# Kernel optimization log

Hardware: AMD Instinct MI355X
Metric: run time of the kernel (lower is better)

Reference implementation:

```python
import jax, jax.numpy as jnp
import numpy as np

B, D_IN, H, HV, A, E, HW = 16384, 512, 512, 256, 32, 8, 512

def _lin(key, fan_in, fan_out):
    k1, k2 = jax.random.split(key)
    s = 1.0 / np.sqrt(fan_in)
    W = jax.random.uniform(k1, (fan_in, fan_out), minval=-s, maxval=s, dtype=jnp.float32)
    b = jax.random.uniform(k2, (fan_out,), minval=-s, maxval=s, dtype=jnp.float32)
    return W, b

def _stack(key, n, fan_in, fan_out):
    Ws, bs = [], []
    for k in jax.random.split(key, n):
        W, b = _lin(k, fan_in, fan_out)
        Ws.append(W); bs.append(b)
    return jnp.stack(Ws), jnp.stack(bs)

def setup_inputs() -> dict:
    key = jax.random.key(0)
    ks = jax.random.split(key, 16)
    x = jax.random.normal(ks[0], (B, D_IN), dtype=jnp.float32)
    # stacked expert policy nets: in->H, H->H, H->A (tanh)
    Wp0, bp0 = _stack(ks[1], E, D_IN, H)
    Wp1, bp1 = _stack(ks[2], E, H, H)
    Wmu, bmu = _stack(ks[3], E, H, A)
    # stacked expert value nets (hardcoded 256 hidden in source): in->256, 256->256, 256->1
    Wv0, bv0 = _stack(ks[4], E, D_IN, HV)
    Wv1, bv1 = _stack(ks[5], E, HV, HV)
    Wv, bv = _stack(ks[6], E, HV, 1)
    # gating net: in->HW, HW->HW, HW->E, softmax
    Ww0, bw0 = _lin(ks[7], D_IN, HW)
    Ww1, bw1 = _lin(ks[8], HW, HW)
    Wwo, bwo = _lin(ks[9], HW, E)
    return dict(x=x, Wp0=Wp0, bp0=bp0, Wp1=Wp1, bp1=bp1, Wmu=Wmu, bmu=bmu,
                Wv0=Wv0, bv0=bv0, Wv1=Wv1, bv1=bv1, Wv=Wv, bv=bv,
                Ww0=Ww0, bw0=bw0, Ww1=Ww1, bw1=bw1, Wwo=Wwo, bwo=bwo)

def reference(x, Wp0, bp0, Wp1, bp1, Wmu, bmu, Wv0, bv0, Wv1, bv1, Wv, bv,
              Ww0, bw0, Ww1, bw1, Wwo, bwo):
    # experts as one grouped/batched GEMM over axis e
    h = jax.nn.relu(jnp.einsum('bi,eih->ebh', x, Wp0) + bp0[:, None, :])      # [E,B,H]
    h = jax.nn.relu(jnp.einsum('ebh,ehk->ebk', h, Wp1) + bp1[:, None, :])
    actions = jnp.tanh(jnp.einsum('ebh,eha->eba', h, Wmu) + bmu[:, None, :])  # [E,B,A]
    # per-expert values
    g = jax.nn.relu(jnp.einsum('bi,eih->ebh', x, Wv0) + bv0[:, None, :])      # [E,B,HV]
    g = jax.nn.relu(jnp.einsum('ebh,ehk->ebk', g, Wv1) + bv1[:, None, :])
    values = jnp.einsum('ebh,eho->ebo', g, Wv) + bv[:, None, :]               # [E,B,1]
    # gating network + softmax
    u = jax.nn.relu(x @ Ww0 + bw0)
    u = jax.nn.relu(u @ Ww1 + bw1)
    w = jax.nn.softmax(u @ Wwo + bwo, axis=-1)                                # [B,E]
    # Categorical(w).sample() with a fixed key, then per-row gather of values
    pis = jax.random.categorical(jax.random.key(42), jnp.log(w), axis=-1)     # [B] int
    v = values[pis, jnp.arange(values.shape[1])]                              # [B,1]
    return actions, v, w
```

## Files before the change

kernel.cpp:

```cpp
#include <hip/hip_runtime.h>


typedef float   f32x4 __attribute__((ext_vector_type(4)));
typedef _Float16 f16;
typedef _Float16 f16x4 __attribute__((ext_vector_type(4)));
typedef _Float16 f16x8 __attribute__((ext_vector_type(8)));

typedef __attribute__((address_space(1))) unsigned int gas_u32;
typedef __attribute__((address_space(3))) unsigned int las_u32;

__device__ __forceinline__ void gl_lds16(const void* g, void* l) {
  __builtin_amdgcn_global_load_lds((gas_u32*)g, (las_u32*)l, 16, 0, 0);
}

__device__ __forceinline__ int xcd_swz(int b, int G) {
  int q = G >> 3, r = G & 7;
  int x = b & 7, y = b >> 3;
  return (x < r ? x * (q + 1) : r * (q + 1) + (x - r) * q) + y;
}

template<int BM, int BN, int WM, int WN, int EPI>
__global__ __launch_bounds__(256, 2) void gemm2_kernel(
    const f16* __restrict__ A, const f16* __restrict__ BT,
    const float* __restrict__ bias, void* __restrict__ Cv,
    const int K, const long long sAe, const long long sCe,
    const int mT, const int nInner, const int eShift)
{
  constexpr int FM = WM / 16, FN = WN / 16;
  constexpr int WAVES_N = BN / WN;
  __shared__ __align__(16) char sm[(BM + BN) * 128];
  char* Ash = sm;
  char* Bsh = sm + BM * 128;

  const int tid = threadIdx.x;
  const int lane = tid & 63;
  const int wid = tid >> 6;

  const int L = xcd_swz(blockIdx.x, gridDim.x);
  const int nIn = L % nInner;
  const int m   = (L / nInner) % mT;
  const int eo  = L / (nInner * mT);
  const int Nreal = 1 << eShift;
  const int nv0 = (eo * nInner + nIn) * BN;
  const int e = nv0 >> eShift;
  const int col0 = nv0 & (Nreal - 1);
  const int m0 = m * BM;

  const f16* Ab = A + (size_t)sAe * e + (size_t)m0 * K;
  const f16* Bb = BT + (size_t)nv0 * K;
  const int wr = wid / WAVES_N, wc = wid % WAVES_N;

  f32x4 acc[FM][FN] = {};

  const int ksteps = K >> 6;
  for (int kt = 0; kt < ksteps; ++kt) {
    __syncthreads();
    const f16* Ak = Ab + (kt << 6);
    const f16* Bk = Bb + (kt << 6);
    for (int u = tid; u < BM * 8; u += 256) {
      int row = u >> 3;
      int kb = ((u & 7) << 4) ^ ((row & 7) << 4);
      gl_lds16(Ak + (size_t)row * K + (kb >> 1), Ash + u * 16);
    }
    for (int u = tid; u < BN * 8; u += 256) {
      int row = u >> 3;
      int kb = ((u & 7) << 4) ^ ((row & 7) << 4);
      gl_lds16(Bk + (size_t)row * K + (kb >> 1), Bsh + u * 16);
    }
    __syncthreads();

    f16x8 af[FM][2], bf[FN][2];
    const int kl = (lane >> 4) << 4;
    #pragma unroll
    for (int fm = 0; fm < FM; ++fm) {
      int row = wr * WM + fm * 16 + (lane & 15);
      int sw = (row & 7) << 4;
      af[fm][0] = *(const f16x8*)(Ash + row * 128 + (kl ^ sw));
      af[fm][1] = *(const f16x8*)(Ash + row * 128 + ((64 + kl) ^ sw));
    }
    #pragma unroll
    for (int fn = 0; fn < FN; ++fn) {
      int row = wc * WN + fn * 16 + (lane & 15);
      int sw = (row & 7) << 4;
      bf[fn][0] = *(const f16x8*)(Bsh + row * 128 + (kl ^ sw));
      bf[fn][1] = *(const f16x8*)(Bsh + row * 128 + ((64 + kl) ^ sw));
    }
    #pragma unroll
    for (int fm = 0; fm < FM; ++fm)
      #pragma unroll
      for (int fn = 0; fn < FN; ++fn) {
        acc[fm][fn] = __builtin_amdgcn_mfma_f32_16x16x32_f16(
            bf[fn][0], af[fm][0], acc[fm][fn], 0, 0, 0);
        acc[fm][fn] = __builtin_amdgcn_mfma_f32_16x16x32_f16(
            bf[fn][1], af[fm][1], acc[fm][fn], 0, 0, 0);
      }
  }

  const int rbase = m0 + wr * WM + (lane & 15);
  const int cb = wc * WN + ((lane >> 4) << 2);
  #pragma unroll
  for (int fm = 0; fm < FM; ++fm) {
    const int row = rbase + fm * 16;
    #pragma unroll
    for (int fn = 0; fn < FN; ++fn) {
      const int bcol = cb + fn * 16;
      f32x4 v = acc[fm][fn];
      f32x4 bb = *(const f32x4*)(bias + nv0 + bcol);
      if constexpr (EPI == 0) {
        f16x4 h;
        #pragma unroll
        for (int r = 0; r < 4; ++r) h[r] = (f16)fmaxf(v[r] + bb[r], 0.0f);
        *(f16x4*)((f16*)Cv + (size_t)sCe * e + (size_t)row * Nreal + col0 + bcol) = h;
      } else {
        f32x4 o;
        #pragma unroll
        for (int r = 0; r < 4; ++r) o[r] = tanhf(v[r] + bb[r]);
        *(f32x4*)((float*)Cv + (size_t)sCe * e + (size_t)row * Nreal + col0 + bcol) = o;
      }
    }
  }
}

__device__ __forceinline__ int swz32(int row) { return ((row >> 1) & 3) << 4; }

__global__ __launch_bounds__(256, 2) void gemm_gate_kernel(
    const f16* __restrict__ Ahi, const f16* __restrict__ Alo,
    const f16* __restrict__ Bhi, const f16* __restrict__ Blo,
    const float* __restrict__ bias,
    f16* __restrict__ Chi, f16* __restrict__ Clo, float* __restrict__ C32,
    const int M, const int N, const int K, const int mode)
{
  constexpr int BM = 128, BN = 128, WM = 64, WN = 64, FM = 4, FN = 4, WAVES_N = 2;
  __shared__ __align__(16) char sm[4 * 128 * 64];
  char* AH = sm;
  char* AL = sm + 8192;
  char* BH = sm + 16384;
  char* BL = sm + 24576;

  const int tid = threadIdx.x;
  const int lane = tid & 63;
  const int wid = tid >> 6;
  const int L = xcd_swz(blockIdx.x, gridDim.x);
  const int ntn = N / BN;
  const int m0 = (L / ntn) * BM;
  const int n0 = (L % ntn) * BN;
  const int wr = wid / WAVES_N, wc = wid % WAVES_N;

  f32x4 a1[FM][FN] = {};
  f32x4 a2[FM][FN] = {};

  const int ksteps = K >> 5;
  for (int kt = 0; kt < ksteps; ++kt) {
    __syncthreads();
    const size_t ko = (size_t)(kt << 5);
    for (int u = tid; u < 512; u += 256) {
      int row = u >> 2;
      int kb = ((u & 3) << 4) ^ swz32(row);
      size_t ga = (size_t)(m0 + row) * K + ko + (kb >> 1);
      size_t gb = (size_t)(n0 + row) * K + ko + (kb >> 1);
      gl_lds16(Ahi + ga, AH + u * 16);
      gl_lds16(Alo + ga, AL + u * 16);
      gl_lds16(Bhi + gb, BH + u * 16);
      gl_lds16(Blo + gb, BL + u * 16);
    }
    __syncthreads();

    f16x8 ah[FM], al[FM], bh[FN], bl[FN];
    const int kl = (lane >> 4) << 4;
    #pragma unroll
    for (int fm = 0; fm < FM; ++fm) {
      int row = wr * WM + fm * 16 + (lane & 15);
      int o = row * 64 + (kl ^ swz32(row));
      ah[fm] = *(const f16x8*)(AH + o);
      al[fm] = *(const f16x8*)(AL + o);
    }
    #pragma unroll
    for (int fn = 0; fn < FN; ++fn) {
      int row = wc * WN + fn * 16 + (lane & 15);
      int o = row * 64 + (kl ^ swz32(row));
      bh[fn] = *(const f16x8*)(BH + o);
      bl[fn] = *(const f16x8*)(BL + o);
    }
    #pragma unroll
    for (int fm = 0; fm < FM; ++fm)
      #pragma unroll
      for (int fn = 0; fn < FN; ++fn) {
        a1[fm][fn] = __builtin_amdgcn_mfma_f32_16x16x32_f16(bh[fn], ah[fm], a1[fm][fn], 0, 0, 0);
        a2[fm][fn] = __builtin_amdgcn_mfma_f32_16x16x32_f16(bh[fn], al[fm], a2[fm][fn], 0, 0, 0);
        a2[fm][fn] = __builtin_amdgcn_mfma_f32_16x16x32_f16(bl[fn], ah[fm], a2[fm][fn], 0, 0, 0);
      }
  }

  const int rbase = m0 + wr * WM + (lane & 15);
  const int cbase = n0 + wc * WN + ((lane >> 4) << 2);
  #pragma unroll
  for (int fm = 0; fm < FM; ++fm) {
    const int row = rbase + fm * 16;
    #pragma unroll
    for (int fn = 0; fn < FN; ++fn) {
      const int col = cbase + fn * 16;
      f32x4 bb = *(const f32x4*)(bias + col);
      if (mode == 0) {
        f16x4 h, l;
        #pragma unroll
        for (int r = 0; r < 4; ++r) {
          float u = fmaxf(a1[fm][fn][r] + a2[fm][fn][r] * 9.765625e-4f + bb[r], 0.0f);
          f16 hh = (f16)u;
          h[r] = hh;
          l[r] = (f16)((u - (float)hh) * 1024.0f);
        }
        *(f16x4*)(Chi + (size_t)row * N + col) = h;
        *(f16x4*)(Clo + (size_t)row * N + col) = l;
      } else {
        f32x4 o;
        #pragma unroll
        for (int r = 0; r < 4; ++r)
          o[r] = fmaxf(a1[fm][fn][r] + a2[fm][fn][r] * 9.765625e-4f + bb[r], 0.0f);
        *(f32x4*)(C32 + (size_t)row * N + col) = o;
      }
    }
  }
}

__global__ __launch_bounds__(256) void cvt_x_kernel(
    const float* __restrict__ x, f16* __restrict__ xhi, f16* __restrict__ xlo)
{
  const size_t i = ((size_t)blockIdx.x * 256 + threadIdx.x) * 4;
  f32x4 v = *(const f32x4*)(x + i);
  f16x4 h, l;
  #pragma unroll
  for (int j = 0; j < 4; ++j) {
    f16 hh = (f16)v[j];
    h[j] = hh;
    l[j] = (f16)((v[j] - (float)hh) * 1024.0f);
  }
  *(f16x4*)(xhi + i) = h;
  *(f16x4*)(xlo + i) = l;
}

__global__ __launch_bounds__(256) void transpose_f16_kernel(
    const float* __restrict__ W, f16* __restrict__ WT, const int K, const int N)
{
  __shared__ float t[32][33];
  const int e = blockIdx.z;
  const int k0 = blockIdx.x << 5, n0 = blockIdx.y << 5;
  const int tx = threadIdx.x & 31, ty = threadIdx.x >> 5;
  const float* Wp = W + (size_t)e * K * N;
  #pragma unroll
  for (int i = 0; i < 4; ++i) {
    int k = k0 + ty + i * 8, n = n0 + tx;
    if (k < K && n < N) t[ty + i * 8][tx] = Wp[(size_t)k * N + n];
  }
  __syncthreads();
  f16* Op = WT + (size_t)e * K * N;
  #pragma unroll
  for (int i = 0; i < 4; ++i) {
    int n = n0 + ty + i * 8, k = k0 + tx;
    if (n < N && k < K) Op[(size_t)n * K + k] = (f16)t[tx][ty + i * 8];
  }
}

__global__ __launch_bounds__(256) void transpose_split_kernel(
    const float* __restrict__ W, f16* __restrict__ Thi, f16* __restrict__ Tlo,
    const int K, const int N)
{
  __shared__ float t[32][33];
  const int k0 = blockIdx.x << 5, n0 = blockIdx.y << 5;
  const int tx = threadIdx.x & 31, ty = threadIdx.x >> 5;
  #pragma unroll
  for (int i = 0; i < 4; ++i) {
    int k = k0 + ty + i * 8, n = n0 + tx;
    if (k < K && n < N) t[ty + i * 8][tx] = W[(size_t)k * N + n];
  }
  __syncthreads();
  #pragma unroll
  for (int i = 0; i < 4; ++i) {
    int n = n0 + ty + i * 8, k = k0 + tx;
    if (n < N && k < K) {
      float v = t[tx][ty + i * 8];
      f16 hh = (f16)v;
      Thi[(size_t)n * K + k] = hh;
      Tlo[(size_t)n * K + k] = (f16)((v - (float)hh) * 1024.0f);
    }
  }
}

__global__ __launch_bounds__(256) void values_kernel(
    const f16* __restrict__ G2, const float* __restrict__ Wv,
    const float* __restrict__ bv, float* __restrict__ values, const int e0)
{
  const int tid = threadIdx.x, lane = tid & 63, wid = tid >> 6;
  const int gi = blockIdx.x * 4 + wid;
  const int el = gi >> 14;
  const int b = gi & 16383;
  const int eg = e0 + el;
  const f16* g = G2 + (((size_t)el << 14) + b) * 256 + (lane << 2);
  f16x4 gv = *(const f16x4*)g;
  const float* wv = Wv + ((size_t)eg << 8) + (lane << 2);
  float a = (float)gv[0] * wv[0] + (float)gv[1] * wv[1] +
            (float)gv[2] * wv[2] + (float)gv[3] * wv[3];
  #pragma unroll
  for (int off = 32; off >= 1; off >>= 1) a += __shfl_xor(a, off);
  if (lane == 0) values[((size_t)eg << 14) + b] = a + bv[eg];
}

__device__ __forceinline__ void threefry_0_42(unsigned x0, unsigned x1,
                                              unsigned& o0, unsigned& o1)
{
  const unsigned ks0 = 0u, ks1 = 42u, ks2 = 0x1BD11BDAu ^ 42u;
  x0 += ks0; x1 += ks1;
#define TF_R(r) { x0 += x1; x1 = (x1 << r) | (x1 >> (32 - r)); x1 ^= x0; }
  TF_R(13) TF_R(15) TF_R(26) TF_R(6)  x0 += ks1; x1 += ks2 + 1u;
  TF_R(17) TF_R(29) TF_R(16) TF_R(24) x0 += ks2; x1 += ks0 + 2u;
  TF_R(13) TF_R(15) TF_R(26) TF_R(6)  x0 += ks0; x1 += ks1 + 3u;
  TF_R(17) TF_R(29) TF_R(16) TF_R(24) x0 += ks1; x1 += ks2 + 4u;
  TF_R(13) TF_R(15) TF_R(26) TF_R(6)  x0 += ks2; x1 += ks0 + 5u;
#undef TF_R
  o0 = x0; o1 = x1;
}

__global__ __launch_bounds__(256) void gating_out_kernel(
    const float* __restrict__ U2, const float* __restrict__ Wwo,
    const float* __restrict__ bwo, const float* __restrict__ values,
    float* __restrict__ w_out, float* __restrict__ v_out)
{
  __shared__ float wl[4096];
  const int tid = threadIdx.x;
  for (int i = tid; i < 1024; i += 256)
    ((f32x4*)wl)[i] = ((const f32x4*)Wwo)[i];
  __syncthreads();
  const int lane = tid & 63, wid = tid >> 6;
  const int b = blockIdx.x * 4 + wid;

  const float* u = U2 + (size_t)b * 512 + lane * 8;
  f32x4 ua = *(const f32x4*)u;
  f32x4 ub = *(const f32x4*)(u + 4);
  float acc[8] = {};
  const float* wrow = wl + lane * 64;
  #pragma unroll
  for (int i = 0; i < 8; ++i) {
    float uv = (i < 4) ? ua[i] : ub[i - 4];
    #pragma unroll
    for (int ee = 0; ee < 8; ++ee) acc[ee] += uv * wrow[i * 8 + ee];
  }
  #pragma unroll
  for (int off = 32; off >= 1; off >>= 1)
    #pragma unroll
    for (int ee = 0; ee < 8; ++ee) acc[ee] += __shfl_xor(acc[ee], off);
  #pragma unroll
  for (int ee = 0; ee < 8; ++ee) acc[ee] += bwo[ee];

  float zmax = acc[0];
  #pragma unroll
  for (int ee = 1; ee < 8; ++ee) zmax = fmaxf(zmax, acc[ee]);
  float s = 0.0f;
  #pragma unroll
  for (int ee = 0; ee < 8; ++ee) s += expf(acc[ee] - zmax);

  float t0 = (lane & 1) ? acc[1] : acc[0];
  float t1 = (lane & 1) ? acc[3] : acc[2];
  float t2 = (lane & 1) ? acc[5] : acc[4];
  float t3 = (lane & 1) ? acc[7] : acc[6];
  float s0 = (lane & 2) ? t1 : t0;
  float s1 = (lane & 2) ? t3 : t2;
  float zown = (lane & 4) ? s1 : s0;

  if (lane < 8) w_out[(size_t)b * 8 + lane] = expf(zown - zmax) / s;

  unsigned idx = ((unsigned)b << 3) | (unsigned)(lane & 7);
  unsigned o0, o1;
  threefry_0_42(0u, idx, o0, o1);
  unsigned bits = o0 ^ o1;
  float f = __uint_as_float((bits >> 9) | 0x3F800000u) - 1.0f;
  f = fmaxf(f, 1.17549435e-38f);
  float g = -logf(-logf(f));
  float y = (lane < 8) ? (zown + g) : -3.0e38f;

  float best = __shfl(y, 0);
  int pi = 0;
  #pragma unroll
  for (int ee = 1; ee < 8; ++ee) {
    float ye = __shfl(y, ee);
    if (ye > best) { best = ye; pi = ee; }
  }
  if (lane == 0) v_out[b] = values[((size_t)pi << 14) + b];
}

extern "C" void kernel_launch(void* const* d_in, const int* in_sizes, int n_in,
                              void* d_out, int out_size, void* d_ws, size_t ws_size,
                              hipStream_t stream) {
  (void)in_sizes; (void)n_in; (void)out_size;
  const float* x   = (const float*)d_in[0];
  const float* Wp0 = (const float*)d_in[1];
  const float* bp0 = (const float*)d_in[2];
  const float* Wp1 = (const float*)d_in[3];
  const float* bp1 = (const float*)d_in[4];
  const float* Wmu = (const float*)d_in[5];
  const float* bmu = (const float*)d_in[6];
  const float* Wv0 = (const float*)d_in[7];
  const float* bv0 = (const float*)d_in[8];
  const float* Wv1 = (const float*)d_in[9];
  const float* bv1 = (const float*)d_in[10];
  const float* Wv  = (const float*)d_in[11];
  const float* bv  = (const float*)d_in[12];
  const float* Ww0 = (const float*)d_in[13];
  const float* bw0 = (const float*)d_in[14];
  const float* Ww1 = (const float*)d_in[15];
  const float* bw1 = (const float*)d_in[16];
  const float* Wwo = (const float*)d_in[17];
  const float* bwo = (const float*)d_in[18];

  float* out_actions = (float*)d_out;
  float* out_v = out_actions + (size_t)8 * 16384 * 32;
  float* out_w = out_v + 16384;

  char* base = (char*)d_ws;
  size_t off = 0;
  auto alloc = [&](size_t bytes) -> char* {
    char* p = base + off;
    off = (off + bytes + 255) & ~(size_t)255;
    return p;
  };

  const size_t BD2 = (size_t)16384 * 512 * 2;
  const size_t BH2 = (size_t)16384 * 256 * 2;

  f16* x16    = (f16*)alloc(BD2);
  f16* xlo    = (f16*)alloc(BD2);
  f16* Wp0T   = (f16*)alloc((size_t)8 * 512 * 512 * 2);
  f16* Wp1T   = (f16*)alloc((size_t)8 * 512 * 512 * 2);
  f16* WmuT   = (f16*)alloc((size_t)8 * 32 * 512 * 2);
  f16* Wv0T   = (f16*)alloc((size_t)8 * 256 * 512 * 2);
  f16* Wv1T   = (f16*)alloc((size_t)8 * 256 * 256 * 2);
  f16* Ww0Thi = (f16*)alloc((size_t)512 * 512 * 2);
  f16* Ww0Tlo = (f16*)alloc((size_t)512 * 512 * 2);
  f16* Ww1Thi = (f16*)alloc((size_t)512 * 512 * 2);
  f16* Ww1Tlo = (f16*)alloc((size_t)512 * 512 * 2);
  float* valuesBuf = (float*)alloc((size_t)8 * 16384 * 4);

  size_t core = off;
  int eg = 8;
  while (eg > 1 && core + (size_t)2 * eg * BD2 > ws_size) eg >>= 1;
  const int eg_v = (2 * eg > 8) ? 8 : 2 * eg;

  f16 *BIG1, *BIG2, *U1hi, *U1lo;
  float* U2;
  if (eg >= 2) {
    BIG1 = (f16*)alloc((size_t)eg * BD2);
    BIG2 = (f16*)alloc((size_t)eg * BD2);
    U1hi = BIG1;
    U1lo = BIG1 + (size_t)16384 * 512;
    U2 = (float*)BIG2;
  } else {
    BIG1 = (f16*)alloc(BD2);
    BIG2 = (f16*)alloc(BD2);
    U1hi = (f16*)alloc(BD2);
    U1lo = (f16*)alloc(BD2);
    U2 = (float*)alloc((size_t)16384 * 512 * 4);
  }
  f16* VB1 = BIG1;
  f16* VB2 = (f16*)((char*)BIG1 + (size_t)eg_v * BH2);

  dim3 blk(256);
  const long long sBD = 16384LL * 512;
  const long long sBH = 16384LL * 256;

  cvt_x_kernel<<<8192, blk, 0, stream>>>(x, x16, xlo);
  transpose_f16_kernel<<<dim3(16, 16, 8), blk, 0, stream>>>(Wp0, Wp0T, 512, 512);
  transpose_f16_kernel<<<dim3(16, 16, 8), blk, 0, stream>>>(Wp1, Wp1T, 512, 512);
  transpose_f16_kernel<<<dim3(16, 1, 8), blk, 0, stream>>>(Wmu, WmuT, 512, 32);
  transpose_f16_kernel<<<dim3(16, 8, 8), blk, 0, stream>>>(Wv0, Wv0T, 512, 256);
  transpose_f16_kernel<<<dim3(8, 8, 8), blk, 0, stream>>>(Wv1, Wv1T, 256, 256);
  transpose_split_kernel<<<dim3(16, 16, 1), blk, 0, stream>>>(Ww0, Ww0Thi, Ww0Tlo, 512, 512);
  transpose_split_kernel<<<dim3(16, 16, 1), blk, 0, stream>>>(Ww1, Ww1Thi, Ww1Tlo, 512, 512);

  for (int e0 = 0; e0 < 8; e0 += eg) {
    gemm2_kernel<128, 128, 64, 64, 0><<<128 * 4 * eg, blk, 0, stream>>>(
        x16, Wp0T + (size_t)e0 * 512 * 512, bp0 + e0 * 512, BIG1,
        512, 0, sBD, 128, 4 * eg, 9);
    gemm2_kernel<128, 128, 64, 64, 0><<<128 * 4 * eg, blk, 0, stream>>>(
        BIG1, Wp1T + (size_t)e0 * 512 * 512, bp1 + e0 * 512, BIG2,
        512, sBD, sBD, 128, 4, 9);
    gemm2_kernel<128, 32, 32, 32, 1><<<128 * eg, blk, 0, stream>>>(
        BIG2, WmuT + (size_t)e0 * 32 * 512, bmu + e0 * 32,
        out_actions + (size_t)e0 * 16384 * 32,
        512, sBD, 16384LL * 32, 128, 1, 5);
  }

  for (int e0 = 0; e0 < 8; e0 += eg_v) {
    gemm2_kernel<128, 128, 64, 64, 0><<<128 * 2 * eg_v, blk, 0, stream>>>(
        x16, Wv0T + (size_t)e0 * 256 * 512, bv0 + e0 * 256, VB1,
        512, 0, sBH, 128, 2 * eg_v, 8);
    gemm2_kernel<128, 128, 64, 64, 0><<<128 * 2 * eg_v, blk, 0, stream>>>(
        VB1, Wv1T + (size_t)e0 * 256 * 256, bv1 + e0 * 256, VB2,
        256, sBH, sBH, 128, 2, 8);
    values_kernel<<<eg_v * 4096, blk, 0, stream>>>((const f16*)VB2, Wv, bv, valuesBuf, e0);
  }

  gemm_gate_kernel<<<512, blk, 0, stream>>>(
      x16, xlo, Ww0Thi, Ww0Tlo, bw0, U1hi, U1lo, nullptr, 16384, 512, 512, 0);
  gemm_gate_kernel<<<512, blk, 0, stream>>>(
      U1hi, U1lo, Ww1Thi, Ww1Tlo, bw1, nullptr, nullptr, U2, 16384, 512, 512, 1);
  gating_out_kernel<<<4096, blk, 0, stream>>>(U2, Wwo, bwo, valuesBuf, out_w, out_v);
}
```

Measured before the change: 466.7 us.

## Add 256x256 eight-wave pipelined GEMM for expert layers and fuse prep kernels

Result: slower. 478.2 us (+2.5%).

```diff
diff --git a/kernel.cpp b/kernel.cpp
--- a/kernel.cpp
+++ b/kernel.cpp
@@ -17,6 +17,118 @@
   int q = G >> 3, r = G & 7;
   int x = b & 7, y = b >> 3;
   return (x < r ? x * (q + 1) : r * (q + 1) + (x - r) * q) + y;
+}
+
+__global__ __launch_bounds__(512, 2) void gemm8_kernel(
+    const f16* __restrict__ A, const f16* __restrict__ BT,
+    const float* __restrict__ bias, f16* __restrict__ C,
+    const int K, const long long sAe, const long long sCe,
+    const int mT, const int nInner, const int eShift)
+{
+  __shared__ __align__(1024) char sm[131072];
+
+  const int tid = threadIdx.x;
+  const int lane = tid & 63;
+  const int wid = tid >> 6;
+  const int wr = wid >> 2, wc = wid & 3;
+  const int kl = (lane >> 4) << 4;
+
+  const int L = xcd_swz(blockIdx.x, gridDim.x);
+  const int nIn = L % nInner;
+  const int m = (L / nInner) % mT;
+  const int eo = L / (nInner * mT);
+  const int Nreal = 1 << eShift;
+  const int nv0 = (eo * nInner + nIn) << 8;
+  const int e = nv0 >> eShift;
+  const int col0 = nv0 & (Nreal - 1);
+  const int m0 = m << 8;
+
+  const f16* Ab = A + (size_t)sAe * e + (size_t)m0 * K;
+  const f16* Bb = BT + (size_t)nv0 * K;
+  const int nt = K >> 6;
+
+  f32x4 acc[8][4] = {};
+
+#define STAGE_A(sp_, ta_, h_) { \
+  char* dst = sm + (((sp_) * 4 + (h_)) << 14); \
+  _Pragma("unroll") for (int i = 0; i < 2; ++i) { \
+    int u = tid + (i << 9); int p = u >> 3; \
+    const char* src = (const char*)(Ab + (size_t)(((p >> 6) << 7) + ((h_) << 6) + (p & 63)) * K) \
+                      + ((size_t)(ta_) << 7) + (((u & 7) << 4) ^ ((p & 7) << 4)); \
+    gl_lds16(src, dst + u * 16); } }
+
+#define STAGE_B(sp_, ta_, h_) { \
+  char* dst = sm + (((sp_) * 4 + 2 + (h_)) << 14); \
+  _Pragma("unroll") for (int i = 0; i < 2; ++i) { \
+    int u = tid + (i << 9); int p = u >> 3; \
+    const char* src = (const char*)(Bb + (size_t)(((p >> 5) << 6) + ((h_) << 5) + (p & 31)) * K) \
+                      + ((size_t)(ta_) << 7) + (((u & 7) << 4) ^ ((p & 7) << 4)); \
+    gl_lds16(src, dst + u * 16); } }
+
+#define VMCNT4 { asm volatile("s_waitcnt vmcnt(4)" ::: "memory"); \
+                 __builtin_amdgcn_sched_barrier(0); }
+
+#define PHASE(t_, mh_, nh_, STAGE_CODE) { \
+  const char* sA = sm + ((((t_) & 1) * 4 + (mh_)) << 14); \
+  const char* sB = sm + ((((t_) & 1) * 4 + 2 + (nh_)) << 14); \
+  f16x8 af[4][2], bf[2][2]; \
+  _Pragma("unroll") for (int fm = 0; fm < 4; ++fm) { \
+    int p = (wr << 6) + (fm << 4) + (lane & 15); int sw = (p & 7) << 4; \
+    af[fm][0] = *(const f16x8*)(sA + p * 128 + (kl ^ sw)); \
+    af[fm][1] = *(const f16x8*)(sA + p * 128 + ((64 + kl) ^ sw)); } \
+  _Pragma("unroll") for (int fn = 0; fn < 2; ++fn) { \
+    int p = (wc << 5) + (fn << 4) + (lane & 15); int sw = (p & 7) << 4; \
+    bf[fn][0] = *(const f16x8*)(sB + p * 128 + (kl ^ sw)); \
+    bf[fn][1] = *(const f16x8*)(sB + p * 128 + ((64 + kl) ^ sw)); } \
+  STAGE_CODE; \
+  __builtin_amdgcn_s_barrier(); \
+  __builtin_amdgcn_s_setprio(1); \
+  _Pragma("unroll") for (int fm = 0; fm < 4; ++fm) \
+  _Pragma("unroll") for (int fn = 0; fn < 2; ++fn) { \
+    acc[(mh_) * 4 + fm][(nh_) * 2 + fn] = __builtin_amdgcn_mfma_f32_16x16x32_f16( \
+        bf[fn][0], af[fm][0], acc[(mh_) * 4 + fm][(nh_) * 2 + fn], 0, 0, 0); \
+    acc[(mh_) * 4 + fm][(nh_) * 2 + fn] = __builtin_amdgcn_mfma_f32_16x16x32_f16( \
+        bf[fn][1], af[fm][1], acc[(mh_) * 4 + fm][(nh_) * 2 + fn], 0, 0, 0); } \
+  __builtin_amdgcn_s_setprio(0); \
+  __builtin_amdgcn_s_barrier(); }
+
+  STAGE_A(0, 0, 0); STAGE_B(0, 0, 0); STAGE_A(0, 0, 1); STAGE_B(0, 0, 1);
+  STAGE_A(1, 1, 0); STAGE_B(1, 1, 0);
+  VMCNT4;
+  __builtin_amdgcn_s_barrier();
+
+  for (int t = 0; t < nt; ++t) {
+    const int tp1 = (t + 1 < nt) ? t + 1 : t;
+    const int tp2 = (t + 2 < nt) ? t + 2 : nt - 1;
+    const int sp1 = (t + 1) & 1, sp0 = t & 1;
+    PHASE(t, 0, 0, STAGE_A(sp1, tp1, 1));
+    PHASE(t, 0, 1, STAGE_B(sp1, tp1, 1));
+    PHASE(t, 1, 0, STAGE_A(sp0, tp2, 0));
+    PHASE(t, 1, 1, STAGE_B(sp0, tp2, 0); VMCNT4);
+  }
+  asm volatile("s_waitcnt vmcnt(0)" ::: "memory");
+
+#undef PHASE
+#undef VMCNT4
+#undef STAGE_A
+#undef STAGE_B
+
+  const int rbase = m0 + (wr << 7) + (lane & 15);
+  const int cb = (wc << 6) + ((lane >> 4) << 2);
+  #pragma unroll
+  for (int fa = 0; fa < 8; ++fa) {
+    const int row = rbase + fa * 16;
+    #pragma unroll
+    for (int fb = 0; fb < 4; ++fb) {
+      const int bcol = cb + fb * 16;
+      f32x4 v = acc[fa][fb];
+      f32x4 bb = *(const f32x4*)(bias + nv0 + bcol);
+      f16x4 h;
+      #pragma unroll
+      for (int r = 0; r < 4; ++r) h[r] = (f16)fmaxf(v[r] + bb[r], 0.0f);
+      *(f16x4*)(C + (size_t)sCe * e + (size_t)row * Nreal + col0 + bcol) = h;
+    }
+  }
 }
 
 template<int BM, int BN, int WM, int WN, int EPI>
@@ -38,8 +150,8 @@
 
   const int L = xcd_swz(blockIdx.x, gridDim.x);
   const int nIn = L % nInner;
-  const int m   = (L / nInner) % mT;
-  const int eo  = L / (nInner * mT);
+  const int m = (L / nInner) % mT;
+  const int eo = L / (nInner * mT);
   const int Nreal = 1 << eShift;
   const int nv0 = (eo * nInner + nIn) * BN;
   const int e = nv0 >> eShift;
@@ -130,7 +242,7 @@
     f16* __restrict__ Chi, f16* __restrict__ Clo, float* __restrict__ C32,
     const int M, const int N, const int K, const int mode)
 {
-  constexpr int BM = 128, BN = 128, WM = 64, WN = 64, FM = 4, FN = 4, WAVES_N = 2;
+  constexpr int FM = 4, FN = 4, WAVES_N = 2;
   __shared__ __align__(16) char sm[4 * 128 * 64];
   char* AH = sm;
   char* AL = sm + 8192;
@@ -141,9 +253,9 @@
   const int lane = tid & 63;
   const int wid = tid >> 6;
   const int L = xcd_swz(blockIdx.x, gridDim.x);
-  const int ntn = N / BN;
-  const int m0 = (L / ntn) * BM;
-  const int n0 = (L % ntn) * BN;
+  const int ntn = N / 128;
+  const int m0 = (L / ntn) * 128;
+  const int n0 = (L % ntn) * 128;
   const int wr = wid / WAVES_N, wc = wid % WAVES_N;
 
   f32x4 a1[FM][FN] = {};
@@ -169,14 +281,14 @@
     const int kl = (lane >> 4) << 4;
     #pragma unroll
     for (int fm = 0; fm < FM; ++fm) {
-      int row = wr * WM + fm * 16 + (lane & 15);
+      int row = wr * 64 + fm * 16 + (lane & 15);
       int o = row * 64 + (kl ^ swz32(row));
       ah[fm] = *(const f16x8*)(AH + o);
       al[fm] = *(const f16x8*)(AL + o);
     }
     #pragma unroll
     for (int fn = 0; fn < FN; ++fn) {
-      int row = wc * WN + fn * 16 + (lane & 15);
+      int row = wc * 64 + fn * 16 + (lane & 15);
       int o = row * 64 + (kl ^ swz32(row));
       bh[fn] = *(const f16x8*)(BH + o);
       bl[fn] = *(const f16x8*)(BL + o);
@@ -191,8 +303,8 @@
       }
   }
 
-  const int rbase = m0 + wr * WM + (lane & 15);
-  const int cbase = n0 + wc * WN + ((lane >> 4) << 2);
+  const int rbase = m0 + wr * 64 + (lane & 15);
+  const int cbase = n0 + wc * 64 + ((lane >> 4) << 2);
   #pragma unroll
   for (int fm = 0; fm < FM; ++fm) {
     const int row = rbase + fm * 16;
@@ -222,66 +334,65 @@
   }
 }
 
-__global__ __launch_bounds__(256) void cvt_x_kernel(
-    const float* __restrict__ x, f16* __restrict__ xhi, f16* __restrict__ xlo)
-{
-  const size_t i = ((size_t)blockIdx.x * 256 + threadIdx.x) * 4;
-  f32x4 v = *(const f32x4*)(x + i);
-  f16x4 h, l;
-  #pragma unroll
-  for (int j = 0; j < 4; ++j) {
-    f16 hh = (f16)v[j];
-    h[j] = hh;
-    l[j] = (f16)((v[j] - (float)hh) * 1024.0f);
-  }
-  *(f16x4*)(xhi + i) = h;
-  *(f16x4*)(xlo + i) = l;
-}
-
-__global__ __launch_bounds__(256) void transpose_f16_kernel(
-    const float* __restrict__ W, f16* __restrict__ WT, const int K, const int N)
+__global__ __launch_bounds__(256) void prep_kernel(
+    const float* __restrict__ x, f16* __restrict__ xhi, f16* __restrict__ xlo,
+    const float* __restrict__ Wp0, f16* __restrict__ Wp0T,
+    const float* __restrict__ Wp1, f16* __restrict__ Wp1T,
+    const float* __restrict__ Wmu, f16* __restrict__ WmuT,
+    const float* __restrict__ Wv0, f16* __restrict__ Wv0T,
+    const float* __restrict__ Wv1, f16* __restrict__ Wv1T,
+    const float* __restrict__ Ww0, f16* __restrict__ Ww0Thi, f16* __restrict__ Ww0Tlo,
+    const float* __restrict__ Ww1, f16* __restrict__ Ww1Thi, f16* __restrict__ Ww1Tlo)
 {
   __shared__ float t[32][33];
-  const int e = blockIdx.z;
-  const int k0 = blockIdx.x << 5, n0 = blockIdx.y << 5;
-  const int tx = threadIdx.x & 31, ty = threadIdx.x >> 5;
+  const int tid = threadIdx.x;
+  int b = blockIdx.x;
+  if (b < 8192) {
+    const size_t i = ((size_t)b * 256 + tid) * 4;
+    f32x4 v = *(const f32x4*)(x + i);
+    f16x4 h, l;
+    #pragma unroll
+    for (int j = 0; j < 4; ++j) {
+      f16 hh = (f16)v[j];
+      h[j] = hh;
+      l[j] = (f16)((v[j] - (float)hh) * 1024.0f);
+    }
+    *(f16x4*)(xhi + i) = h;
+    *(f16x4*)(xlo + i) = l;
+    return;
+  }
+  b -= 8192;
+  const float* W;
+  f16* T;
+  f16* T2 = nullptr;
+  int K, N;
+  if (b < 2048)               { W = Wp0; T = Wp0T; K = 512; N = 512; }
+  else if ((b -= 2048) < 2048){ W = Wp1; T = Wp1T; K = 512; N = 512; }
+  else if ((b -= 2048) < 128) { W = Wmu; T = WmuT; K = 512; N = 32; }
+  else if ((b -= 128) < 1024) { W = Wv0; T = Wv0T; K = 512; N = 256; }
+  else if ((b -= 1024) < 512) { W = Wv1; T = Wv1T; K = 256; N = 256; }
+  else if ((b -= 512) < 256)  { W = Ww0; T = Ww0Thi; T2 = Ww0Tlo; K = 512; N = 512; }
+  else { b -= 256;              W = Ww1; T = Ww1Thi; T2 = Ww1Tlo; K = 512; N = 512; }
+
+  const int kT = K >> 5, nT = N >> 5;
+  const int e = b / (kT * nT);
+  const int rem = b % (kT * nT);
+  const int k0 = (rem % kT) << 5;
+  const int n0 = (rem / kT) << 5;
+  const int tx = tid & 31, ty = tid >> 5;
   const float* Wp = W + (size_t)e * K * N;
   #pragma unroll
+  for (int i = 0; i < 4; ++i)
+    t[ty + i * 8][tx] = Wp[(size_t)(k0 + ty + i * 8) * N + n0 + tx];
+  __syncthreads();
+  f16* Op = T + (size_t)e * K * N;
+  #pragma unroll
   for (int i = 0; i < 4; ++i) {
-    int k = k0 + ty + i * 8, n = n0 + tx;
-    if (k < K && n < N) t[ty + i * 8][tx] = Wp[(size_t)k * N + n];
-  }
-  __syncthreads();
-  f16* Op = WT + (size_t)e * K * N;
-  #pragma unroll
-  for (int i = 0; i < 4; ++i) {
-    int n = n0 + ty + i * 8, k = k0 + tx;
-    if (n < N && k < K) Op[(size_t)n * K + k] = (f16)t[tx][ty + i * 8];
-  }
-}
-
-__global__ __launch_bounds__(256) void transpose_split_kernel(
-    const float* __restrict__ W, f16* __restrict__ Thi, f16* __restrict__ Tlo,
-    const int K, const int N)
-{
-  __shared__ float t[32][33];
-  const int k0 = blockIdx.x << 5, n0 = blockIdx.y << 5;
-  const int tx = threadIdx.x & 31, ty = threadIdx.x >> 5;
-  #pragma unroll
-  for (int i = 0; i < 4; ++i) {
-    int k = k0 + ty + i * 8, n = n0 + tx;
-    if (k < K && n < N) t[ty + i * 8][tx] = W[(size_t)k * N + n];
-  }
-  __syncthreads();
-  #pragma unroll
-  for (int i = 0; i < 4; ++i) {
-    int n = n0 + ty + i * 8, k = k0 + tx;
-    if (n < N && k < K) {
-      float v = t[tx][ty + i * 8];
-      f16 hh = (f16)v;
-      Thi[(size_t)n * K + k] = hh;
-      Tlo[(size_t)n * K + k] = (f16)((v - (float)hh) * 1024.0f);
-    }
+    const int n = n0 + ty + i * 8, k = k0 + tx;
+    float v = t[tx][ty + i * 8];
+    f16 hh = (f16)v;
+    Op[(size_t)n * K + k] = hh;
+    if (T2) T2[(size_t)n * K + k] = (f16)((v - (float)hh) * 1024.0f);
   }
 }
 
@@ -462,25 +573,21 @@
   f16* VB2 = (f16*)((char*)BIG1 + (size_t)eg_v * BH2);
 
   dim3 blk(256);
+  dim3 blk8(512);
   const long long sBD = 16384LL * 512;
   const long long sBH = 16384LL * 256;
 
-  cvt_x_kernel<<<8192, blk, 0, stream>>>(x, x16, xlo);
-  transpose_f16_kernel<<<dim3(16, 16, 8), blk, 0, stream>>>(Wp0, Wp0T, 512, 512);
-  transpose_f16_kernel<<<dim3(16, 16, 8), blk, 0, stream>>>(Wp1, Wp1T, 512, 512);
-  transpose_f16_kernel<<<dim3(16, 1, 8), blk, 0, stream>>>(Wmu, WmuT, 512, 32);
-  transpose_f16_kernel<<<dim3(16, 8, 8), blk, 0, stream>>>(Wv0, Wv0T, 512, 256);
-  transpose_f16_kernel<<<dim3(8, 8, 8), blk, 0, stream>>>(Wv1, Wv1T, 256, 256);
-  transpose_split_kernel<<<dim3(16, 16, 1), blk, 0, stream>>>(Ww0, Ww0Thi, Ww0Tlo, 512, 512);
-  transpose_split_kernel<<<dim3(16, 16, 1), blk, 0, stream>>>(Ww1, Ww1Thi, Ww1Tlo, 512, 512);
+  prep_kernel<<<14464, blk, 0, stream>>>(
+      x, x16, xlo, Wp0, Wp0T, Wp1, Wp1T, Wmu, WmuT, Wv0, Wv0T, Wv1, Wv1T,
+      Ww0, Ww0Thi, Ww0Tlo, Ww1, Ww1Thi, Ww1Tlo);
 
   for (int e0 = 0; e0 < 8; e0 += eg) {
-    gemm2_kernel<128, 128, 64, 64, 0><<<128 * 4 * eg, blk, 0, stream>>>(
+    gemm8_kernel<<<64 * 2 * eg, blk8, 0, stream>>>(
         x16, Wp0T + (size_t)e0 * 512 * 512, bp0 + e0 * 512, BIG1,
-        512, 0, sBD, 128, 4 * eg, 9);
-    gemm2_kernel<128, 128, 64, 64, 0><<<128 * 4 * eg, blk, 0, stream>>>(
+        512, 0, sBD, 64, 2 * eg, 9);
+    gemm8_kernel<<<64 * 2 * eg, blk8, 0, stream>>>(
         BIG1, Wp1T + (size_t)e0 * 512 * 512, bp1 + e0 * 512, BIG2,
-        512, sBD, sBD, 128, 4, 9);
+        512, sBD, sBD, 64, 2, 9);
     gemm2_kernel<128, 32, 32, 32, 1><<<128 * eg, blk, 0, stream>>>(
         BIG2, WmuT + (size_t)e0 * 32 * 512, bmu + e0 * 32,
         out_actions + (size_t)e0 * 16384 * 32,
@@ -488,12 +595,12 @@
   }
 
   for (int e0 = 0; e0 < 8; e0 += eg_v) {
-    gemm2_kernel<128, 128, 64, 64, 0><<<128 * 2 * eg_v, blk, 0, stream>>>(
+    gemm8_kernel<<<64 * eg_v, blk8, 0, stream>>>(
         x16, Wv0T + (size_t)e0 * 256 * 512, bv0 + e0 * 256, VB1,
-        512, 0, sBH, 128, 2 * eg_v, 8);
-    gemm2_kernel<128, 128, 64, 64, 0><<<128 * 2 * eg_v, blk, 0, stream>>>(
+        512, 0, sBH, 64, eg_v, 8);
+    gemm8_kernel<<<64 * eg_v, blk8, 0, stream>>>(
         VB1, Wv1T + (size_t)e0 * 256 * 256, bv1 + e0 * 256, VB2,
-        256, sBH, sBH, 128, 2, 8);
+        256, sBH, sBH, 64, 1, 8);
     values_kernel<<<eg_v * 4096, blk, 0, stream>>>((const f16*)VB2, Wv, bv, valuesBuf, e0);
   }
 
```
